# Performance work log

Hardware: AMD Instinct MI355X
Metric: run time of the kernel (lower is better)

The kernel has to match this reference:

```python
import jax, jax.numpy as jnp
import numpy as np

B, T, M = 32, 1024, 40
CD, H, C = 128, 256, 10  # conv_dims, rnn_hidden_dims, num_classes
DN = ('NCHW', 'OIHW', 'NCHW')


def _conv_block(x, W, b, pool):
    # 3x3 'same' conv + ReLU + max-pool (1, pool) over the mel axis
    y = jax.lax.conv_general_dilated(x, W, (1, 1), 'SAME', dimension_numbers=DN)
    y = jax.nn.relu(y + b[None, :, None, None])
    return jax.lax.reduce_window(y, -jnp.inf, jax.lax.max,
                                 (1, 1, 1, pool), (1, 1, 1, pool), 'VALID')


def setup_inputs() -> dict:
    key = jax.random.key(0)
    ks = jax.random.split(key, 12)
    inp = {}
    inp['x'] = jax.random.normal(ks[0], (B, 1, T, M), dtype=jnp.float32)
    inp['targets'] = (jax.random.uniform(ks[1], (B, T, C)) > 0.5).astype(jnp.float32)
    inp['force_mask'] = jax.random.randint(ks[2], (T, B), 0, 2, dtype=jnp.int32)
    s = 0.05
    inp['W1'] = jax.random.normal(ks[3], (CD, 1, 3, 3), dtype=jnp.float32) * s
    inp['b1'] = jnp.zeros((CD,), jnp.float32)
    inp['W2'] = jax.random.normal(ks[4], (CD, CD, 3, 3), dtype=jnp.float32) * s
    inp['b2'] = jnp.zeros((CD,), jnp.float32)
    inp['W3'] = jax.random.normal(ks[5], (CD, CD, 3, 3), dtype=jnp.float32) * s
    inp['b3'] = jnp.zeros((CD,), jnp.float32)
    inp['W_ih'] = jax.random.normal(ks[6], (3 * H, CD + C), dtype=jnp.float32) * s
    inp['W_hh'] = jax.random.normal(ks[7], (3 * H, H), dtype=jnp.float32) * s
    inp['b_ih'] = jnp.zeros((3 * H,), jnp.float32)
    inp['b_hh'] = jnp.zeros((3 * H,), jnp.float32)
    inp['Wf'] = jax.random.normal(ks[8], (C, H), dtype=jnp.float32) * s
    inp['bf'] = jnp.zeros((C,), jnp.float32)
    return inp


def reference(x, targets, force_mask, W1, b1, W2, b2, W3, b3,
              W_ih, W_hh, b_ih, b_hh, Wf, bf):
    # CNN feature extractor: mel axis 40 -> 8 -> 2 -> 1
    f = _conv_block(x, W1, b1, 5)
    f = _conv_block(f, W2, b2, 4)
    f = _conv_block(f, W3, b3, 2)          # [B, CD, T, 1]
    feats = f[..., 0].transpose(2, 0, 1)    # [T, B, CD]
    tgt_t = targets.transpose(1, 0, 2)       # [T, B, C]

    def step(carry, inp_t):
        h, tf = carry
        xt, tg, fm = inp_t                  # [B,CD], [B,C], [B]
        xc = jnp.concatenate([xt, tf], axis=-1)
        gi = xc @ W_ih.T + b_ih
        gh = h @ W_hh.T + b_hh
        i_r, i_z, i_n = jnp.split(gi, 3, axis=-1)
        h_r, h_z, h_n = jnp.split(gh, 3, axis=-1)
        r = jax.nn.sigmoid(i_r + h_r)
        z = jax.nn.sigmoid(i_z + h_z)
        n = jnp.tanh(i_n + r * h_n)
        h_new = (1.0 - z) * n + z * h
        out = h_new @ Wf.T + bf             # [B, C]
        pred = (jax.nn.sigmoid(out) > 0.5).astype(out.dtype)
        tf_new = jnp.where(fm[:, None] > 0, tg, pred)
        return (h_new, tf_new), out

    h0 = jnp.zeros((B, H), x.dtype)
    tf0 = jnp.zeros((B, C), x.dtype)
    _, outs = jax.lax.scan(step, (h0, tf0), (feats, tgt_t, force_mask))
    return outs.transpose(1, 0, 2)          # [B, T, C]
```

## Files before the change

kernel.cpp:

```cpp
#include <hip/hip_runtime.h>
#include <math.h>

#define B_ 32
#define T_ 1024
#define M_ 40

__global__ void prep_kernel(const float* __restrict__ W_hh, const float* __restrict__ W2,
                            const float* __restrict__ W3, const float* __restrict__ W_ih,
                            float* __restrict__ WhhT, float* __restrict__ W2t,
                            float* __restrict__ W3t, float* __restrict__ WihT4) {
  int idx = blockIdx.x * 256 + threadIdx.x;
  if (idx < 196608) {
    int k = idx / 768, j = idx % 768;
    WhhT[idx] = W_hh[j * 256 + k];
    return;
  }
  idx -= 196608;
  if (idx < 147456) {
    int tap = idx >> 14, ci = (idx >> 7) & 127, co = idx & 127;
    W2t[idx] = W2[(co * 128 + ci) * 9 + tap];
    return;
  }
  idx -= 147456;
  if (idx < 147456) {
    int tap = idx >> 14, ci = (idx >> 7) & 127, co = idx & 127;
    W3t[idx] = W3[(co * 128 + ci) * 9 + tap];
    return;
  }
  idx -= 147456;
  if (idx < 98304) {
    int khi = idx / 3072, rem = idx % 3072, j = rem >> 2, klo = rem & 3;
    WihT4[idx] = W_ih[j * 138 + khi * 4 + klo];
  }
}

__global__ __launch_bounds__(256) void conv12_kernel(
    const float* __restrict__ x, const float* __restrict__ W1, const float* __restrict__ b1,
    const float* __restrict__ W2t, const float* __restrict__ b2, float* __restrict__ y2) {
  __shared__ float xt[8 * 42];
  __shared__ float y1s[6 * 128 * 12];
  const int tid = threadIdx.x;
  const int t0 = blockIdx.x * 4;
  const int b = blockIdx.y;
  for (int idx = tid; idx < 8 * 42; idx += 256) {
    int row = idx / 42, slot = idx % 42;
    int t_in = t0 - 2 + row, m = slot - 1;
    float v = 0.f;
    if (t_in >= 0 && t_in < T_ && m >= 0 && m < M_) v = x[(b * T_ + t_in) * M_ + m];
    xt[idx] = v;
  }
  __syncthreads();
  const int c = tid & 127, q = tid >> 7;
  float w1[9];
#pragma unroll
  for (int i = 0; i < 9; ++i) w1[i] = W1[c * 9 + i];
  const float b1c = b1[c];
  for (int rr = 0; rr < 3; ++rr) {
    const int r = q * 3 + rr;
    const int t_in = t0 - 1 + r;
    float* yrow = &y1s[(r * 128 + c) * 12];
    if (t_in < 0 || t_in >= T_) {
#pragma unroll
      for (int s = 0; s < 12; ++s) yrow[s] = 0.f;
    } else {
      yrow[0] = 0.f; yrow[9] = 0.f; yrow[10] = 0.f; yrow[11] = 0.f;
#pragma unroll
      for (int mo = 0; mo < 8; ++mo) {
        float mx = -1e30f;
#pragma unroll
        for (int i5 = 0; i5 < 5; ++i5) {
          const int mp = mo * 5 + i5;
          float s = b1c;
#pragma unroll
          for (int dt = 0; dt < 3; ++dt)
#pragma unroll
            for (int dm = 0; dm < 3; ++dm)
              s += xt[(r + dt) * 42 + mp + dm] * w1[dt * 3 + dm];
          mx = fmaxf(mx, s);
        }
        yrow[1 + mo] = fmaxf(mx, 0.f);
      }
    }
  }
  __syncthreads();
  const int co = c, tq = q;
  float acc[2][8];
#pragma unroll
  for (int tl = 0; tl < 2; ++tl)
#pragma unroll
    for (int mo = 0; mo < 8; ++mo) acc[tl][mo] = 0.f;
  for (int ci = 0; ci < 128; ++ci) {
    float w[9];
#pragma unroll
    for (int i = 0; i < 9; ++i) w[i] = W2t[i * 16384 + ci * 128 + co];
    float xv[4][10];
#pragma unroll
    for (int rr = 0; rr < 4; ++rr) {
      const float* p = &y1s[((2 * tq + rr) * 128 + ci) * 12];
      const float4 a = *(const float4*)p;
      const float4 bq = *(const float4*)(p + 4);
      const float2 cq = *(const float2*)(p + 8);
      xv[rr][0] = a.x; xv[rr][1] = a.y; xv[rr][2] = a.z; xv[rr][3] = a.w;
      xv[rr][4] = bq.x; xv[rr][5] = bq.y; xv[rr][6] = bq.z; xv[rr][7] = bq.w;
      xv[rr][8] = cq.x; xv[rr][9] = cq.y;
    }
#pragma unroll
    for (int dt = 0; dt < 3; ++dt)
#pragma unroll
      for (int dm = 0; dm < 3; ++dm) {
        const float wv = w[dt * 3 + dm];
#pragma unroll
        for (int tl = 0; tl < 2; ++tl)
#pragma unroll
          for (int mo = 0; mo < 8; ++mo)
            acc[tl][mo] += xv[tl + dt][mo + dm] * wv;
      }
  }
  const float b2c = b2[co];
#pragma unroll
  for (int tl = 0; tl < 2; ++tl) {
    const int t = t0 + 2 * tq + tl;
    float m0 = fmaxf(fmaxf(acc[tl][0], acc[tl][1]), fmaxf(acc[tl][2], acc[tl][3])) + b2c;
    float m1 = fmaxf(fmaxf(acc[tl][4], acc[tl][5]), fmaxf(acc[tl][6], acc[tl][7])) + b2c;
    y2[((b * T_ + t) * 2 + 0) * 128 + co] = fmaxf(m0, 0.f);
    y2[((b * T_ + t) * 2 + 1) * 128 + co] = fmaxf(m1, 0.f);
  }
}

__global__ __launch_bounds__(256) void conv3_kernel(
    const float* __restrict__ y2, const float* __restrict__ W3t, const float* __restrict__ b3,
    float* __restrict__ feats) {
  __shared__ float y2s[6 * 128 * 4];
  const int tid = threadIdx.x;
  const int t0 = blockIdx.x * 4;
  const int b = blockIdx.y;
  for (int idx = tid; idx < 768; idx += 256) {
    int row = idx / 128, ci = idx % 128;
    y2s[(row * 128 + ci) * 4 + 0] = 0.f;
    y2s[(row * 128 + ci) * 4 + 3] = 0.f;
  }
  for (int idx = tid; idx < 6 * 256; idx += 256) {
    int row = idx / 256, rem = idx % 256;
    int m = rem >> 7, ci = rem & 127;
    int t_in = t0 - 1 + row;
    float v = 0.f;
    if (t_in >= 0 && t_in < T_) v = y2[((b * T_ + t_in) * 2 + m) * 128 + ci];
    y2s[(row * 128 + ci) * 4 + 1 + m] = v;
  }
  __syncthreads();
  const int co = tid & 127, tq = tid >> 7;
  float acc[2][2] = {{0.f, 0.f}, {0.f, 0.f}};
  for (int ci = 0; ci < 128; ++ci) {
    float w[9];
#pragma unroll
    for (int i = 0; i < 9; ++i) w[i] = W3t[i * 16384 + ci * 128 + co];
    float4 xr[4];
#pragma unroll
    for (int rr = 0; rr < 4; ++rr)
      xr[rr] = *(const float4*)&y2s[((2 * tq + rr) * 128 + ci) * 4];
#pragma unroll
    for (int dt = 0; dt < 3; ++dt)
#pragma unroll
      for (int tl = 0; tl < 2; ++tl) {
        const float4 v = xr[tl + dt];
        acc[tl][0] += v.y * w[dt * 3 + 1] + v.z * w[dt * 3 + 2];
        acc[tl][1] += v.y * w[dt * 3 + 0] + v.z * w[dt * 3 + 1];
      }
  }
  const float b3c = b3[co];
#pragma unroll
  for (int tl = 0; tl < 2; ++tl) {
    const int t = t0 + 2 * tq + tl;
    float f = fmaxf(fmaxf(acc[tl][0], acc[tl][1]) + b3c, 0.f);
    feats[(t * B_ + b) * 128 + co] = f;
  }
}

__global__ __launch_bounds__(256) void gid_kernel(
    const float* __restrict__ feats, const float* __restrict__ WihT4,
    const float* __restrict__ b_ih, float* __restrict__ gi) {
  __shared__ float fs[32 * 128];
  const int tid = threadIdx.x;
  const int jb = blockIdx.x;
  const int rb = blockIdx.y;
  const float4* src = (const float4*)(feats + rb * 32 * 128);
  float4* dst = (float4*)fs;
  for (int i = tid; i < 1024; i += 256) dst[i] = src[i];
  __syncthreads();
  const int j = jb * 256 + tid;
  float acc[32];
#pragma unroll
  for (int r = 0; r < 32; ++r) acc[r] = 0.f;
  for (int k4 = 0; k4 < 32; ++k4) {
    const float4 w4 = *(const float4*)&WihT4[(k4 * 768 + j) * 4];
#pragma unroll
    for (int r = 0; r < 32; ++r) {
      const float4 f4 = *(const float4*)&fs[r * 128 + k4 * 4];
      acc[r] += f4.x * w4.x + f4.y * w4.y + f4.z * w4.z + f4.w * w4.w;
    }
  }
  const float bj = b_ih[j];
  for (int r = 0; r < 32; ++r) gi[(rb * 32 + r) * 768 + j] = acc[r] + bj;
}

__global__ __launch_bounds__(768) void rnn_kernel(
    const float* __restrict__ gi, const float* __restrict__ WhhT,
    const float* __restrict__ W_ih, const float* __restrict__ b_hh,
    const float* __restrict__ Wf, const float* __restrict__ bf,
    const float* __restrict__ targets, const int* __restrict__ force_mask,
    float* __restrict__ out) {
  __shared__ float Wl[2 * 8 * 1536];
  __shared__ float h_s[256];
  __shared__ float tf_s[16];
  __shared__ float gis[768];
  __shared__ float part[4 * 768];
  __shared__ float wtf[10 * 768];
  __shared__ float wfs[10 * 256];
  __shared__ float bhh_s[768];
  __shared__ float bf_s[16];
  const int tid = threadIdx.x;
  const int b = blockIdx.x;
  for (int idx = tid; idx < 7680; idx += 768) {
    int cc = idx / 768, j = idx % 768;
    wtf[idx] = W_ih[j * 138 + 128 + cc];
  }
  for (int idx = tid; idx < 2560; idx += 768) wfs[idx] = Wf[idx];
  bhh_s[tid] = b_hh[tid];
  if (tid < 256) h_s[tid] = 0.f;
  if (tid < 10) { tf_s[tid] = 0.f; bf_s[tid] = bf[tid]; }
  const int ks = tid / 192;
  const int jq = tid % 192;
  const float* wbase = WhhT + (ks * 64) * 768 + jq * 4;
  float4 wr[6][4];
#pragma unroll
  for (int g = 0; g < 6; ++g) {
    const float* wp0 = wbase + g * 3072;
    wr[g][0] = *(const float4*)(wp0);
    wr[g][1] = *(const float4*)(wp0 + 768);
    wr[g][2] = *(const float4*)(wp0 + 1536);
    wr[g][3] = *(const float4*)(wp0 + 2304);
  }
#pragma unroll
  for (int gg = 0; gg < 2; ++gg) {
    const float* src = wbase + (6 + gg) * 3072;
#pragma unroll
    for (int fp = 0; fp < 8; ++fp) {
      const int f0 = 2 * fp, f1 = 2 * fp + 1;
      Wl[(gg * 8 + fp) * 1536 + tid * 2 + 0] = src[(f0 >> 2) * 768 + (f0 & 3)];
      Wl[(gg * 8 + fp) * 1536 + tid * 2 + 1] = src[(f1 >> 2) * 768 + (f1 & 3)];
    }
  }
  __syncthreads();
  for (int t = 0; t < T_; ++t) {
    float giv = gi[(t * B_ + b) * 768 + tid];
#pragma unroll
    for (int cc = 0; cc < 10; ++cc) giv += wtf[cc * 768 + tid] * tf_s[cc];
    float4 a4 = make_float4(0.f, 0.f, 0.f, 0.f);
#pragma unroll
    for (int g = 0; g < 6; ++g) {
      const float4 h4 = *(const float4*)&h_s[ks * 64 + g * 4];
      a4.x += wr[g][0].x * h4.x + wr[g][1].x * h4.y + wr[g][2].x * h4.z + wr[g][3].x * h4.w;
      a4.y += wr[g][0].y * h4.x + wr[g][1].y * h4.y + wr[g][2].y * h4.z + wr[g][3].y * h4.w;
      a4.z += wr[g][0].z * h4.x + wr[g][1].z * h4.y + wr[g][2].z * h4.z + wr[g][3].z * h4.w;
      a4.w += wr[g][0].w * h4.x + wr[g][1].w * h4.y + wr[g][2].w * h4.z + wr[g][3].w * h4.w;
    }
#pragma unroll
    for (int gg = 0; gg < 2; ++gg) {
      const float4 h4 = *(const float4*)&h_s[ks * 64 + (6 + gg) * 4];
      const float* base = &Wl[(gg * 8) * 1536 + tid * 2];
      const float2 p0 = *(const float2*)(base);
      const float2 p1 = *(const float2*)(base + 1536);
      const float2 p2 = *(const float2*)(base + 3072);
      const float2 p3 = *(const float2*)(base + 4608);
      const float2 p4 = *(const float2*)(base + 6144);
      const float2 p5 = *(const float2*)(base + 7680);
      const float2 p6 = *(const float2*)(base + 9216);
      const float2 p7 = *(const float2*)(base + 10752);
      a4.x += p0.x * h4.x + p2.x * h4.y + p4.x * h4.z + p6.x * h4.w;
      a4.y += p0.y * h4.x + p2.y * h4.y + p4.y * h4.z + p6.y * h4.w;
      a4.z += p1.x * h4.x + p3.x * h4.y + p5.x * h4.z + p7.x * h4.w;
      a4.w += p1.y * h4.x + p3.y * h4.y + p5.y * h4.z + p7.y * h4.w;
    }
    const float* wp = wbase + 8 * 3072;
#pragma unroll 2
    for (int g8 = 8; g8 < 16; ++g8) {
      const float4 w0 = *(const float4*)(wp);
      const float4 w1v = *(const float4*)(wp + 768);
      const float4 w2v = *(const float4*)(wp + 1536);
      const float4 w3v = *(const float4*)(wp + 2304);
      const float4 h4 = *(const float4*)&h_s[ks * 64 + g8 * 4];
      a4.x += w0.x * h4.x + w1v.x * h4.y + w2v.x * h4.z + w3v.x * h4.w;
      a4.y += w0.y * h4.x + w1v.y * h4.y + w2v.y * h4.z + w3v.y * h4.w;
      a4.z += w0.z * h4.x + w1v.z * h4.y + w2v.z * h4.z + w3v.z * h4.w;
      a4.w += w0.w * h4.x + w1v.w * h4.y + w2v.w * h4.z + w3v.w * h4.w;
      wp += 3072;
    }
    *(float4*)&part[ks * 768 + jq * 4] = a4;
    gis[tid] = giv;
    __syncthreads();
    if (tid < 256) {
      const int j = tid;
      float ghr = bhh_s[j] + part[j] + part[768 + j] + part[1536 + j] + part[2304 + j];
      float ghz = bhh_s[256 + j] + part[256 + j] + part[1024 + j] + part[1792 + j] + part[2560 + j];
      float ghn = bhh_s[512 + j] + part[512 + j] + part[1280 + j] + part[2048 + j] + part[2816 + j];
      const float r = 1.f / (1.f + expf(-(gis[j] + ghr)));
      const float z = 1.f / (1.f + expf(-(gis[256 + j] + ghz)));
      const float n = tanhf(gis[512 + j] + r * ghn);
      h_s[j] = (1.f - z) * n + z * h_s[j];
    }
    __syncthreads();
    if (tid < 64) {
      const float h0 = h_s[tid], h1 = h_s[tid + 64], h2 = h_s[tid + 128], h3 = h_s[tid + 192];
      float p[10];
#pragma unroll
      for (int cc = 0; cc < 10; ++cc)
        p[cc] = wfs[cc * 256 + tid] * h0 + wfs[cc * 256 + tid + 64] * h1 +
                wfs[cc * 256 + tid + 128] * h2 + wfs[cc * 256 + tid + 192] * h3;
#pragma unroll
      for (int off = 32; off > 0; off >>= 1)
#pragma unroll
        for (int cc = 0; cc < 10; ++cc) p[cc] += __shfl_xor(p[cc], off);
      if (tid == 0) {
        const int fm = force_mask[t * B_ + b];
#pragma unroll
        for (int cc = 0; cc < 10; ++cc) {
          const float o = p[cc] + bf_s[cc];
          out[(b * T_ + t) * 10 + cc] = o;
          tf_s[cc] = (fm > 0) ? targets[(b * T_ + t) * 10 + cc] : (o > 0.f ? 1.f : 0.f);
        }
      }
    }
    __syncthreads();
  }
}

extern "C" void kernel_launch(void* const* d_in, const int* in_sizes, int n_in,
                              void* d_out, int out_size, void* d_ws, size_t ws_size,
                              hipStream_t stream) {
  const float* x = (const float*)d_in[0];
  const float* targets = (const float*)d_in[1];
  const int* fmask = (const int*)d_in[2];
  const float* W1 = (const float*)d_in[3];
  const float* b1 = (const float*)d_in[4];
  const float* W2 = (const float*)d_in[5];
  const float* b2 = (const float*)d_in[6];
  const float* W3 = (const float*)d_in[7];
  const float* b3 = (const float*)d_in[8];
  const float* Wih = (const float*)d_in[9];
  const float* Whh = (const float*)d_in[10];
  const float* bih = (const float*)d_in[11];
  const float* bhh = (const float*)d_in[12];
  const float* Wf = (const float*)d_in[13];
  const float* bf = (const float*)d_in[14];
  float* out = (float*)d_out;
  float* ws = (float*)d_ws;
  float* WhhT = ws;
  float* W2t = ws + 196608;
  float* W3t = ws + 344064;
  float* WihT4 = ws + 491520;
  float* feats = ws + 589824;
  float* gi = ws + 4784128;
  float* y2 = gi;

  prep_kernel<<<2304, 256, 0, stream>>>(Whh, W2, W3, Wih, WhhT, W2t, W3t, WihT4);
  conv12_kernel<<<dim3(256, 32), 256, 0, stream>>>(x, W1, b1, W2t, b2, y2);
  conv3_kernel<<<dim3(256, 32), 256, 0, stream>>>(y2, W3t, b3, feats);
  gid_kernel<<<dim3(3, 1024), 256, 0, stream>>>(feats, WihT4, bih, gi);
  rnn_kernel<<<32, 768, 0, stream>>>(gi, WhhT, Wih, bhh, Wf, bf, targets, fmask, out);
}
```

Baseline: 8.001 ms.

## Overlap next-step hidden matvec with output head and prefetch targets

Restructures the GRU time loop so the recurrent matvec for step t+1 runs right after the gate update, concurrently with the output projection and teacher-forcing on thread 0. The teacher-forcing contribution to the input gates moves out of the matvec and into the gate-update threads. This removes one block-wide barrier per step. Thread 0 also prefetches the next step's force mask and targets into registers to hide global load latency. It adds launch_bounds min-blocks of 3, which may constrain register allocation and cause spills.

```diff
diff --git a/kernel.cpp b/kernel.cpp
--- a/kernel.cpp
+++ b/kernel.cpp
@@ -203,7 +203,7 @@
   for (int r = 0; r < 32; ++r) gi[(rb * 32 + r) * 768 + j] = acc[r] + bj;
 }
 
-__global__ __launch_bounds__(768) void rnn_kernel(
+__global__ __launch_bounds__(768, 3) void rnn_kernel(
     const float* __restrict__ gi, const float* __restrict__ WhhT,
     const float* __restrict__ W_ih, const float* __restrict__ b_hh,
     const float* __restrict__ Wf, const float* __restrict__ bf,
@@ -251,10 +251,9 @@
     }
   }
   __syncthreads();
-  for (int t = 0; t < T_; ++t) {
-    float giv = gi[(t * B_ + b) * 768 + tid];
-#pragma unroll
-    for (int cc = 0; cc < 10; ++cc) giv += wtf[cc * 768 + tid] * tf_s[cc];
+
+  auto matvec = [&](int tt) {
+    float giv = gi[(tt * B_ + b) * 768 + tid];
     float4 a4 = make_float4(0.f, 0.f, 0.f, 0.f);
 #pragma unroll
     for (int g = 0; g < 6; ++g) {
@@ -297,15 +296,35 @@
     }
     *(float4*)&part[ks * 768 + jq * 4] = a4;
     gis[tid] = giv;
-    __syncthreads();
+  };
+
+  int fm_r = 0;
+  float tg_r[10];
+  if (tid == 0) {
+    fm_r = force_mask[0 * B_ + b];
+#pragma unroll
+    for (int cc = 0; cc < 10; ++cc) tg_r[cc] = targets[(b * T_ + 0) * 10 + cc];
+  }
+  matvec(0);
+  __syncthreads();
+
+  for (int t = 0; t < T_; ++t) {
     if (tid < 256) {
       const int j = tid;
+      float gr = gis[j], gz = gis[256 + j], gn0 = gis[512 + j];
+#pragma unroll
+      for (int cc = 0; cc < 10; ++cc) {
+        const float tfv = tf_s[cc];
+        gr += wtf[cc * 768 + j] * tfv;
+        gz += wtf[cc * 768 + 256 + j] * tfv;
+        gn0 += wtf[cc * 768 + 512 + j] * tfv;
+      }
       float ghr = bhh_s[j] + part[j] + part[768 + j] + part[1536 + j] + part[2304 + j];
       float ghz = bhh_s[256 + j] + part[256 + j] + part[1024 + j] + part[1792 + j] + part[2560 + j];
       float ghn = bhh_s[512 + j] + part[512 + j] + part[1280 + j] + part[2048 + j] + part[2816 + j];
-      const float r = 1.f / (1.f + expf(-(gis[j] + ghr)));
-      const float z = 1.f / (1.f + expf(-(gis[256 + j] + ghz)));
-      const float n = tanhf(gis[512 + j] + r * ghn);
+      const float r = 1.f / (1.f + expf(-(gr + ghr)));
+      const float z = 1.f / (1.f + expf(-(gz + ghz)));
+      const float n = tanhf(gn0 + r * ghn);
       h_s[j] = (1.f - z) * n + z * h_s[j];
     }
     __syncthreads();
@@ -321,15 +340,20 @@
 #pragma unroll
         for (int cc = 0; cc < 10; ++cc) p[cc] += __shfl_xor(p[cc], off);
       if (tid == 0) {
-        const int fm = force_mask[t * B_ + b];
 #pragma unroll
         for (int cc = 0; cc < 10; ++cc) {
           const float o = p[cc] + bf_s[cc];
           out[(b * T_ + t) * 10 + cc] = o;
-          tf_s[cc] = (fm > 0) ? targets[(b * T_ + t) * 10 + cc] : (o > 0.f ? 1.f : 0.f);
+          tf_s[cc] = (fm_r > 0) ? tg_r[cc] : (o > 0.f ? 1.f : 0.f);
         }
-      }
-    }
+        if (t + 1 < T_) {
+          fm_r = force_mask[(t + 1) * B_ + b];
+#pragma unroll
+          for (int cc = 0; cc < 10; ++cc) tg_r[cc] = targets[(b * T_ + t + 1) * 10 + cc];
+        }
+      }
+    }
+    if (t + 1 < T_) matvec(t + 1);
     __syncthreads();
   }
 }
```

Result: faster. 7.231 ms (-9.6%).
